# Kernel optimization log

Hardware: AMD Instinct MI355X
Metric: run time of the kernel (lower is better)

The kernel has to match this reference:

```python
import jax, jax.numpy as jnp
import numpy as np

B, C, D, H, W = 4, 1, 192, 192, 192
SMALL = 4            # int(192 * bias_scale=0.025)
BIAS_STD = 0.7
MAX_SIGMA = 3.0
TRUNCATE = 4.0
K = 2 * int(TRUNCATE * MAX_SIGMA) + 1   # fixed truncated kernel size = 25
N_LABELS = 32
TABLE = 128          # static remap-table size (>= max source label, >= max dest)


def setup_inputs() -> dict:
    key = jax.random.key(0)
    k1, k2, k3, k4, k5 = jax.random.split(key, 5)
    return {
        "x": jax.random.normal(k1, (B, C, D, H, W), jnp.float32),
        "small_bias": jax.random.normal(k2, (B, 1, SMALL, SMALL, SMALL), jnp.float32),
        "sigma01": jax.random.uniform(k3, (B, 3), jnp.float32),
        "labels": jax.random.randint(k4, (B, 1, D, H, W), 0, N_LABELS, jnp.int32),
        "source_values": jnp.arange(N_LABELS, dtype=jnp.int64),
        "dest_values": jax.random.randint(k5, (N_LABELS,), 0, 100, jnp.int64),
    }


def _lin_weights(n_in, n_out):
    """Dense 1D linear-interp matrix [n_out, n_in], align_corners=True."""
    pos = jnp.linspace(0.0, n_in - 1.0, n_out)
    i0 = jnp.clip(jnp.floor(pos).astype(jnp.int32), 0, n_in - 2)
    f = pos - i0.astype(pos.dtype)
    r = jnp.arange(n_out)
    Wm = jnp.zeros((n_out, n_in), jnp.float32)
    Wm = Wm.at[r, i0].add(1.0 - f).at[r, i0 + 1].add(f)
    return Wm


def _bias_field(small_bias):
    # trilinear align_corners upsample [B,1,s,s,s] -> [B,1,D,H,W], separable
    b = small_bias * BIAS_STD
    b = jnp.einsum('bcxyz,dx->bcdyz', b, _lin_weights(SMALL, D))
    b = jnp.einsum('bcdyz,hy->bcdhz', b, _lin_weights(SMALL, H))
    b = jnp.einsum('bcdhz,wz->bcdhw', b, _lin_weights(SMALL, W))
    return b


def _gauss_kernels(sigma):
    """sigma [3] -> normalized kernels [3, K]; identity (delta) where sigma<0.01."""
    ar = jnp.arange(K, dtype=jnp.float32) - K // 2
    s = jnp.maximum(sigma, 1e-3)[:, None]
    g = jnp.exp(-0.5 * (ar[None, :] ** 2) / (s ** 2))
    g = g / g.sum(-1, keepdims=True)
    delta = jnp.zeros((K,), jnp.float32).at[K // 2].set(1.0)
    return jnp.where(sigma[:, None] >= 0.01, g, delta[None, :])


def _blur_axis(x, k, axis):
    # x [C,D,H,W]; depthwise 1D conv along `axis` with replicate (edge) padding
    p = K // 2
    xm = jnp.moveaxis(x, axis, -1)
    shp = xm.shape
    xm = xm.reshape(-1, 1, shp[-1])
    xm = jnp.pad(xm, ((0, 0), (0, 0), (p, p)), mode='edge')
    out = jax.lax.conv_general_dilated(xm, k.reshape(1, 1, K), (1,), 'VALID')
    return jnp.moveaxis(out.reshape(shp), -1, axis)


def _blur_sample(x, kernels):
    # x [C,D,H,W], kernels [3,K]; separable blur over D,H,W
    for i, ax in enumerate((1, 2, 3)):
        x = _blur_axis(x, kernels[i], ax)
    return x


def reference(x, small_bias, sigma01, labels, source_values, dest_values):
    # 1) bias-field corruption: x * exp(upsampled random field)
    img = x * jnp.exp(_bias_field(small_bias))
    # 2) dynamic per-sample Gaussian blur, sigma in [0, MAX_SIGMA]
    kernels = jax.vmap(_gauss_kernels)(sigma01 * MAX_SIGMA)   # [B,3,K]
    img = jax.vmap(_blur_sample)(img, kernels)
    # 3) label remap via lookup table gather
    mapping = jnp.zeros((TABLE,), jnp.int32).at[source_values].set(
        dest_values.astype(jnp.int32))
    labels_out = mapping[labels]
    return img, labels_out
```

## Files before the change

kernel.cpp:

```cpp
#include <hip/hip_runtime.h>
#include <hip/hip_fp16.h>
#include <cstdint>
#include <cstddef>

#define Bc 4
#define Dd 192
#define Hh 192
#define Ww 192
#define KK 25
#define RR 12
#define VOL (Bc*Dd*Hh*Ww)
#define SP 216
#define SPU (SP/2)
#define SH 98
#define RIN 120

typedef unsigned short u16;
typedef unsigned int   u32;

__global__ void setup_tables_kernel(const float* __restrict__ sigma01,
                                    const int* __restrict__ src,
                                    const int* __restrict__ dst,
                                    float* __restrict__ kern,
                                    u32* __restrict__ kern2,
                                    int* __restrict__ mapping) {
    int t = threadIdx.x;
    if (t < 128) mapping[t] = 0;
    __syncthreads();
    if (t < 32) {
        int s = src[t];
        if (s >= 0 && s < 128) mapping[s] = dst[t];
    }
    if (t < Bc * 3) {
        float sig = sigma01[t] * 3.0f;
        float s = fmaxf(sig, 1e-3f);
        float g[KK];
        float sum = 0.0f;
        #pragma unroll
        for (int i = 0; i < KK; i++) {
            float a = (float)(i - RR);
            float v = expf(-0.5f * a * a / (s * s));
            g[i] = v; sum += v;
        }
        float inv = 1.0f / sum;
        #pragma unroll
        for (int i = 0; i < KK; i++) {
            float v = g[i] * inv;
            if (sig < 0.01f) v = (i == RR) ? 1.0f : 0.0f;
            kern[t * KK + i] = v;
            u16 hb = __builtin_bit_cast(u16, __float2half(v));
            kern2[t * KK + i] = (u32)hb | ((u32)hb << 16);
        }
    }
}

__global__ __launch_bounds__(512) void pass_wh_remap_kernel(
    const float* __restrict__ x, u16* __restrict__ outB,
    const u32* __restrict__ kern2,
    const float* __restrict__ sb,
    const int4* __restrict__ labels, float4* __restrict__ lab_out,
    const int* __restrict__ mapping) {
    __shared__ u16 P[RIN * SP];
    __shared__ __attribute__((aligned(16))) float ch[RIN][4];
    const int tid = threadIdx.x;
    const int hx = blockIdx.x;
    const int d  = blockIdx.y;
    const int b  = blockIdx.z;

    if (tid < RIN) {
        int r = tid;
        int hrow = min(max(96 * hx - RR + r, 0), Hh - 1);
        float pos_d = d * (3.0f / 191.0f);
        int   id0   = min((int)pos_d, 2);
        float fd    = pos_d - (float)id0;
        float pos_h = hrow * (3.0f / 191.0f);
        int   ih0   = min((int)pos_h, 2);
        float fh    = pos_h - (float)ih0;
        const float* sbA = sb + b * 64 + id0 * 16 + ih0 * 4;
        #pragma unroll
        for (int k = 0; k < 4; k++) {
            float v00 = sbA[k],      v01 = sbA[4 + k];
            float v10 = sbA[16 + k], v11 = sbA[20 + k];
            float vd0 = (1.f - fd) * v00 + fd * v10;
            float vd1 = (1.f - fd) * v01 + fd * v11;
            ch[r][k] = ((1.f - fh) * vd0 + fh * vd1) * 0.7f;
        }
    }
    __syncthreads();

    const size_t pbase = ((size_t)b * Dd + d) * (size_t)(Hh * Ww);
    #pragma unroll
    for (int it = 0; it < 12; it++) {
        int i4 = it * 512 + tid;
        if (i4 < RIN * 48) {
            int r = i4 / 48, w4 = i4 % 48;
            int w = 4 * w4;
            int hrow = min(max(96 * hx - RR + r, 0), Hh - 1);
            float4 v = *(const float4*)(x + pbase + (size_t)hrow * Ww + w);
            float4 cv = *(const float4*)&ch[r][0];
            float rs[4];
            #pragma unroll
            for (int j = 0; j < 4; j++) {
                float pw = (w + j) * (3.0f / 191.0f);
                bool s1 = pw >= 1.0f, s2 = pw >= 2.0f;
                float clo = s2 ? cv.z : (s1 ? cv.y : cv.x);
                float chi = s2 ? cv.w : (s1 ? cv.z : cv.y);
                float fb  = s2 ? 2.0f : (s1 ? 1.0f : 0.0f);
                float fw  = pw - fb;
                float bias = clo + fw * (chi - clo);
                float val = (j == 0 ? v.x : j == 1 ? v.y : j == 2 ? v.z : v.w);
                rs[j] = val * __expf(bias);
            }
            u32 p0 = (u32)__builtin_bit_cast(u16, __float2half(rs[0])) |
                     ((u32)__builtin_bit_cast(u16, __float2half(rs[1])) << 16);
            u32 p1 = (u32)__builtin_bit_cast(u16, __float2half(rs[2])) |
                     ((u32)__builtin_bit_cast(u16, __float2half(rs[3])) << 16);
            u32* dstp = (u32*)&P[r * SP + RR + w];
            dstp[0] = p0; dstp[1] = p1;
            if (w4 == 0) {
                u16 hv = __builtin_bit_cast(u16, __float2half(rs[0]));
                u32 hh = (u32)hv | ((u32)hv << 16);
                u32* hp = (u32*)&P[r * SP];
                #pragma unroll
                for (int m = 0; m < 6; m++) hp[m] = hh;
            } else if (w4 == 47) {
                u16 hv = __builtin_bit_cast(u16, __float2half(rs[3]));
                u32 hh = (u32)hv | ((u32)hv << 16);
                u32* hp = (u32*)&P[r * SP + RR + Ww];
                #pragma unroll
                for (int m = 0; m < 6; m++) hp[m] = hh;
            }
        }
    }
    __syncthreads();

    {
        const u32* kw2 = kern2 + (b * 3 + 2) * KK;
        const int wv = tid >> 6, ln = tid & 63;
        const int r4 = ln >> 4;
        const int c  = ln & 15;
        #pragma unroll
        for (int it = 0; it < 4; it++) {
            const int lr = it * 4 + r4;
            if (lr < 15) {
                const int row = wv * 15 + lr;
                const u32* rp = (const u32*)P + row * SPU + 6 * c;
                u32 E[18];
                #pragma unroll
                for (int j = 0; j < 18; j++) E[j] = rp[j];
                u32 O[17];
                #pragma unroll
                for (int j = 0; j < 17; j++)
                    O[j] = (E[j] >> 16) | (E[j + 1] << 16);
                __half2 acc[6];
                #pragma unroll
                for (int m = 0; m < 6; m++) acc[m] = __float2half2_rn(0.0f);
                #pragma unroll
                for (int s = 0; s < 13; s++) {
                    __half2 kv = __builtin_bit_cast(__half2, kw2[2 * s]);
                    #pragma unroll
                    for (int m = 0; m < 6; m++)
                        acc[m] = __hfma2(kv, __builtin_bit_cast(__half2, E[m + s]), acc[m]);
                }
                #pragma unroll
                for (int s = 0; s < 12; s++) {
                    __half2 kv = __builtin_bit_cast(__half2, kw2[2 * s + 1]);
                    #pragma unroll
                    for (int m = 0; m < 6; m++)
                        acc[m] = __hfma2(kv, __builtin_bit_cast(__half2, O[m + s]), acc[m]);
                }
                u32* wp = (u32*)P + row * SPU + 6 + 6 * c;
                #pragma unroll
                for (int m = 0; m < 6; m++)
                    wp[m] = __builtin_bit_cast(u32, acc[m]);
            }
        }
    }
    __syncthreads();

    {
        const u32* kh2 = kern2 + (b * 3 + 1) * KK;
        u32* outp = (u32*)(outB + pbase);
        #pragma unroll
        for (int it = 0; it < 2; it++) {
            int item = it * 512 + tid;
            if (item < 768) {
                int col = item % 96;
                int g = item / 96;
                u32 win[36];
                #pragma unroll
                for (int i = 0; i < 36; i++)
                    win[i] = *((const u32*)P + (g * 12 + i) * SPU + 6 + col);
                __half2 acc[12];
                #pragma unroll
                for (int j = 0; j < 12; j++) acc[j] = __float2half2_rn(0.0f);
                #pragma unroll
                for (int t = 0; t < KK; t++) {
                    __half2 kv = __builtin_bit_cast(__half2, kh2[t]);
                    #pragma unroll
                    for (int j = 0; j < 12; j++)
                        acc[j] = __hfma2(kv, __builtin_bit_cast(__half2, win[j + t]), acc[j]);
                }
                #pragma unroll
                for (int j = 0; j < 12; j++)
                    outp[(96 * hx + g * 12 + j) * 96 + col] =
                        __builtin_bit_cast(u32, acc[j]);
            }
        }
    }

    {
        const int bid = ((b * Dd) + d) * 2 + hx;
        int base = bid * 4608 + tid;
        #pragma unroll
        for (int it = 0; it < 9; it++) {
            int i = base + it * 512;
            int4 l = labels[i];
            float4 o;
            o.x = (float)mapping[min(max(l.x, 0), 127)];
            o.y = (float)mapping[min(max(l.y, 0), 127)];
            o.z = (float)mapping[min(max(l.z, 0), 127)];
            o.w = (float)mapping[min(max(l.w, 0), 127)];
            lab_out[i] = o;
        }
    }
}

__global__ __launch_bounds__(192) void pass_d_kernel(
    const u16* __restrict__ in, float* __restrict__ img,
    const u32* __restrict__ kern2) {
    __shared__ __attribute__((aligned(16))) u16 T[88 * SH];
    const int tid = threadIdx.x;
    const int w0 = blockIdx.x * 96;
    const int d0 = blockIdx.y * 64;
    const int z = blockIdx.z;
    const int h = z % Hh, b = z / Hh;
    const u32* kp = kern2 + b * 3 * KK;
    #pragma unroll
    for (int k = 0; k < 6; k++) {
        int idx = k * 192 + tid;
        if (idx < 1056) {
            int r = idx / 12, sg = idx % 12;
            int dd = min(max(d0 + r - RR, 0), Dd - 1);
            uint4 v = *(const uint4*)(in + (((size_t)b * Dd + dd) * Hh + h) * (size_t)Ww + w0 + sg * 8);
            u32* p = (u32*)&T[r * SH + sg * 8];
            p[0] = v.x; p[1] = v.y; p[2] = v.z; p[3] = v.w;
        }
    }
    __syncthreads();
    const int p = tid % 48;
    const int g0 = tid / 48;
    #pragma unroll
    for (int cc = 0; cc < 2; cc++) {
        const int g = g0 + cc * 4;
        const int ob = g * 8;
        u32 win[32];
        #pragma unroll
        for (int i = 0; i < 32; i++) win[i] = *(const u32*)&T[(ob + i) * SH + 2 * p];
        __half2 acc[8];
        #pragma unroll
        for (int j = 0; j < 8; j++) acc[j] = __float2half2_rn(0.0f);
        #pragma unroll
        for (int t = 0; t < KK; t++) {
            __half2 kv = __builtin_bit_cast(__half2, kp[t]);
            #pragma unroll
            for (int j = 0; j < 8; j++)
                acc[j] = __hfma2(kv, __builtin_bit_cast(__half2, win[j + t]), acc[j]);
        }
        #pragma unroll
        for (int j = 0; j < 8; j++) {
            float2 f = __half22float2(acc[j]);
            *(float2*)(img + (((size_t)b * Dd + (d0 + ob + j)) * Hh + h) * (size_t)Ww + w0 + 2 * p) = f;
        }
    }
}

extern "C" void kernel_launch(void* const* d_in, const int* in_sizes, int n_in,
                              void* d_out, int out_size, void* d_ws, size_t ws_size,
                              hipStream_t stream) {
    const float* x          = (const float*)d_in[0];
    const float* small_bias = (const float*)d_in[1];
    const float* sigma01    = (const float*)d_in[2];
    const int*   labels     = (const int*)d_in[3];
    const int*   src        = (const int*)d_in[4];
    const int*   dst        = (const int*)d_in[5];

    float* out     = (float*)d_out;
    float* img     = out;
    float* lab_out = out + (size_t)VOL;

    float* kern    = (float*)d_ws;
    u32*   kern2   = (u32*)((float*)d_ws + 384);
    int*   mapping = (int*)((float*)d_ws + 768);
    u16*   Bb      = (u16*)((char*)d_ws + 8192);

    setup_tables_kernel<<<1, 128, 0, stream>>>(sigma01, src, dst, kern, kern2, mapping);

    pass_wh_remap_kernel<<<dim3(2, Dd, Bc), 512, 0, stream>>>(
        x, Bb, kern2, small_bias,
        (const int4*)labels, (float4*)lab_out, mapping);
    pass_d_kernel<<<dim3(Ww / 96, Dd / 64, Bc * Hh), 192, 0, stream>>>(Bb, img, kern2);
}
```

Before: 141.2 us.

## Move label remap into D pass and retile WH pass to 64-row blocks

The label remap moves out of the W/H blur kernel into the D-pass kernel, which now reads a float copy of the mapping table from shared memory. The W/H kernel is retiled from 2 blocks of 96 output rows with 512 threads to 3 blocks of 64 rows with 256 threads, and its inner loops are adjusted to match. The aim is to balance work between the two kernels and raise occupancy in the W/H pass. In exchange, the 12-row halo is recomputed more often, so more redundant x loads and bias exps happen per output row.

```diff
diff --git a/kernel.cpp b/kernel.cpp
--- a/kernel.cpp
+++ b/kernel.cpp
@@ -13,7 +13,7 @@
 #define SP 216
 #define SPU (SP/2)
 #define SH 98
-#define RIN 120
+#define RIN 88
 
 typedef unsigned short u16;
 typedef unsigned int   u32;
@@ -23,7 +23,8 @@
                                     const int* __restrict__ dst,
                                     float* __restrict__ kern,
                                     u32* __restrict__ kern2,
-                                    int* __restrict__ mapping) {
+                                    int* __restrict__ mapping,
+                                    float* __restrict__ mapf) {
     int t = threadIdx.x;
     if (t < 128) mapping[t] = 0;
     __syncthreads();
@@ -31,6 +32,8 @@
         int s = src[t];
         if (s >= 0 && s < 128) mapping[s] = dst[t];
     }
+    __syncthreads();
+    if (t < 128) mapf[t] = (float)mapping[t];
     if (t < Bc * 3) {
         float sig = sigma01[t] * 3.0f;
         float s = fmaxf(sig, 1e-3f);
@@ -54,12 +57,10 @@
     }
 }
 
-__global__ __launch_bounds__(512) void pass_wh_remap_kernel(
+__global__ __launch_bounds__(256) void pass_wh_kernel(
     const float* __restrict__ x, u16* __restrict__ outB,
     const u32* __restrict__ kern2,
-    const float* __restrict__ sb,
-    const int4* __restrict__ labels, float4* __restrict__ lab_out,
-    const int* __restrict__ mapping) {
+    const float* __restrict__ sb) {
     __shared__ u16 P[RIN * SP];
     __shared__ __attribute__((aligned(16))) float ch[RIN][4];
     const int tid = threadIdx.x;
@@ -69,7 +70,7 @@
 
     if (tid < RIN) {
         int r = tid;
-        int hrow = min(max(96 * hx - RR + r, 0), Hh - 1);
+        int hrow = min(max(64 * hx - RR + r, 0), Hh - 1);
         float pos_d = d * (3.0f / 191.0f);
         int   id0   = min((int)pos_d, 2);
         float fd    = pos_d - (float)id0;
@@ -90,12 +91,12 @@
 
     const size_t pbase = ((size_t)b * Dd + d) * (size_t)(Hh * Ww);
     #pragma unroll
-    for (int it = 0; it < 12; it++) {
-        int i4 = it * 512 + tid;
+    for (int it = 0; it < 17; it++) {
+        int i4 = it * 256 + tid;
         if (i4 < RIN * 48) {
             int r = i4 / 48, w4 = i4 % 48;
             int w = 4 * w4;
-            int hrow = min(max(96 * hx - RR + r, 0), Hh - 1);
+            int hrow = min(max(64 * hx - RR + r, 0), Hh - 1);
             float4 v = *(const float4*)(x + pbase + (size_t)hrow * Ww + w);
             float4 cv = *(const float4*)&ch[r][0];
             float rs[4];
@@ -140,10 +141,10 @@
         const int r4 = ln >> 4;
         const int c  = ln & 15;
         #pragma unroll
-        for (int it = 0; it < 4; it++) {
+        for (int it = 0; it < 6; it++) {
             const int lr = it * 4 + r4;
-            if (lr < 15) {
-                const int row = wv * 15 + lr;
+            if (lr < 22) {
+                const int row = wv * 22 + lr;
                 const u32* rp = (const u32*)P + row * SPU + 6 * c;
                 u32 E[18];
                 #pragma unroll
@@ -182,60 +183,46 @@
         const u32* kh2 = kern2 + (b * 3 + 1) * KK;
         u32* outp = (u32*)(outB + pbase);
         #pragma unroll
-        for (int it = 0; it < 2; it++) {
-            int item = it * 512 + tid;
-            if (item < 768) {
-                int col = item % 96;
-                int g = item / 96;
-                u32 win[36];
-                #pragma unroll
-                for (int i = 0; i < 36; i++)
-                    win[i] = *((const u32*)P + (g * 12 + i) * SPU + 6 + col);
-                __half2 acc[12];
-                #pragma unroll
-                for (int j = 0; j < 12; j++) acc[j] = __float2half2_rn(0.0f);
-                #pragma unroll
-                for (int t = 0; t < KK; t++) {
-                    __half2 kv = __builtin_bit_cast(__half2, kh2[t]);
-                    #pragma unroll
-                    for (int j = 0; j < 12; j++)
-                        acc[j] = __hfma2(kv, __builtin_bit_cast(__half2, win[j + t]), acc[j]);
-                }
-                #pragma unroll
-                for (int j = 0; j < 12; j++)
-                    outp[(96 * hx + g * 12 + j) * 96 + col] =
-                        __builtin_bit_cast(u32, acc[j]);
+        for (int it = 0; it < 3; it++) {
+            int item = it * 256 + tid;
+            int col = item % 96;
+            int g = item / 96;
+            u32 win[32];
+            #pragma unroll
+            for (int i = 0; i < 32; i++)
+                win[i] = *((const u32*)P + (g * 8 + i) * SPU + 6 + col);
+            __half2 acc[8];
+            #pragma unroll
+            for (int j = 0; j < 8; j++) acc[j] = __float2half2_rn(0.0f);
+            #pragma unroll
+            for (int t = 0; t < KK; t++) {
+                __half2 kv = __builtin_bit_cast(__half2, kh2[t]);
+                #pragma unroll
+                for (int j = 0; j < 8; j++)
+                    acc[j] = __hfma2(kv, __builtin_bit_cast(__half2, win[j + t]), acc[j]);
             }
-        }
-    }
-
-    {
-        const int bid = ((b * Dd) + d) * 2 + hx;
-        int base = bid * 4608 + tid;
-        #pragma unroll
-        for (int it = 0; it < 9; it++) {
-            int i = base + it * 512;
-            int4 l = labels[i];
-            float4 o;
-            o.x = (float)mapping[min(max(l.x, 0), 127)];
-            o.y = (float)mapping[min(max(l.y, 0), 127)];
-            o.z = (float)mapping[min(max(l.z, 0), 127)];
-            o.w = (float)mapping[min(max(l.w, 0), 127)];
-            lab_out[i] = o;
+            #pragma unroll
+            for (int j = 0; j < 8; j++)
+                outp[(64 * hx + g * 8 + j) * 96 + col] =
+                    __builtin_bit_cast(u32, acc[j]);
         }
     }
 }
 
-__global__ __launch_bounds__(192) void pass_d_kernel(
+__global__ __launch_bounds__(192) void pass_d_remap_kernel(
     const u16* __restrict__ in, float* __restrict__ img,
-    const u32* __restrict__ kern2) {
+    const u32* __restrict__ kern2,
+    const int4* __restrict__ labels, float4* __restrict__ lab_out,
+    const float* __restrict__ mapf) {
     __shared__ __attribute__((aligned(16))) u16 T[88 * SH];
+    __shared__ float Lmap[128];
     const int tid = threadIdx.x;
     const int w0 = blockIdx.x * 96;
     const int d0 = blockIdx.y * 64;
     const int z = blockIdx.z;
     const int h = z % Hh, b = z / Hh;
     const u32* kp = kern2 + b * 3 * KK;
+    if (tid < 128) Lmap[tid] = mapf[tid];
     #pragma unroll
     for (int k = 0; k < 6; k++) {
         int idx = k * 192 + tid;
@@ -273,6 +260,21 @@
             *(float2*)(img + (((size_t)b * Dd + (d0 + ob + j)) * Hh + h) * (size_t)Ww + w0 + 2 * p) = f;
         }
     }
+    {
+        const int bid = (z * 3 + blockIdx.y) * 2 + blockIdx.x;
+        int base = bid * 1536 + tid;
+        #pragma unroll
+        for (int it = 0; it < 8; it++) {
+            int i = base + it * 192;
+            int4 l = labels[i];
+            float4 o;
+            o.x = Lmap[min(max(l.x, 0), 127)];
+            o.y = Lmap[min(max(l.y, 0), 127)];
+            o.z = Lmap[min(max(l.z, 0), 127)];
+            o.w = Lmap[min(max(l.w, 0), 127)];
+            lab_out[i] = o;
+        }
+    }
 }
 
 extern "C" void kernel_launch(void* const* d_in, const int* in_sizes, int n_in,
@@ -292,12 +294,13 @@
     float* kern    = (float*)d_ws;
     u32*   kern2   = (u32*)((float*)d_ws + 384);
     int*   mapping = (int*)((float*)d_ws + 768);
+    float* mapf    = (float*)d_ws + 896;
     u16*   Bb      = (u16*)((char*)d_ws + 8192);
 
-    setup_tables_kernel<<<1, 128, 0, stream>>>(sigma01, src, dst, kern, kern2, mapping);
-
-    pass_wh_remap_kernel<<<dim3(2, Dd, Bc), 512, 0, stream>>>(
-        x, Bb, kern2, small_bias,
-        (const int4*)labels, (float4*)lab_out, mapping);
-    pass_d_kernel<<<dim3(Ww / 96, Dd / 64, Bc * Hh), 192, 0, stream>>>(Bb, img, kern2);
+    setup_tables_kernel<<<1, 128, 0, stream>>>(sigma01, src, dst, kern, kern2,
+                                               mapping, mapf);
+
+    pass_wh_kernel<<<dim3(3, Dd, Bc), 256, 0, stream>>>(x, Bb, kern2, small_bias);
+    pass_d_remap_kernel<<<dim3(Ww / 96, Dd / 64, Bc * Hh), 192, 0, stream>>>(
+        Bb, img, kern2, (const int4*)labels, (float4*)lab_out, mapf);
 }
```

Result: slower. 154.1 us (+9.1%).
